# Optimization experiments

Measured on AMD Instinct MI355X. Metric: run time of the kernel, lower is better.

## Reference

```python
import jax, jax.numpy as jnp
import numpy as np

BN_EPS = 1e-5


def setup_inputs() -> dict:
    key = jax.random.key(0)
    ks = jax.random.split(key, 6)
    B, N, M, C1, C2 = 8, 8192, 2048, 128, 256
    in_ch = C1 + C2  # 384
    return {
        "xyz1": jax.random.uniform(ks[0], (B, N, 3), dtype=jnp.float32),
        "xyz2": jax.random.uniform(ks[1], (B, M, 3), dtype=jnp.float32),
        "features1": jax.random.normal(ks[2], (B, C1, N), dtype=jnp.float32),
        "features2": jax.random.normal(ks[3], (B, C2, M), dtype=jnp.float32),
        # Conv1d(kernel_size=1, bias=False) weights, squeezed to [out, in]
        "conv_w0": jax.random.normal(ks[4], (256, in_ch), dtype=jnp.float32) * 0.05,
        "gamma0": jnp.ones((256,), dtype=jnp.float32),
        "beta0": jnp.zeros((256,), dtype=jnp.float32),
        "conv_w1": jax.random.normal(ks[5], (256, 256), dtype=jnp.float32) * 0.05,
        "gamma1": jnp.ones((256,), dtype=jnp.float32),
        "beta1": jnp.zeros((256,), dtype=jnp.float32),
    }


def _conv_bn_relu(x, w, gamma, beta):
    # 1x1 Conv1d (no bias) == per-point channel matmul: [B,Cin,N] -> [B,Cout,N]
    x = jnp.einsum("oc,bcn->bon", w, x)
    # BatchNorm1d in training mode: batch stats over (B, N), biased variance
    mu = jnp.mean(x, axis=(0, 2), keepdims=True)
    var = jnp.var(x, axis=(0, 2), keepdims=True)
    x = (x - mu) * jax.lax.rsqrt(var + BN_EPS)
    x = x * gamma[None, :, None] + beta[None, :, None]
    return jax.nn.relu(x)


def reference(xyz1, xyz2, features1, features2,
              conv_w0, gamma0, beta0, conv_w1, gamma1, beta1):
    # squared pairwise distances [B, N, M] (broadcast diff reduced over coord dim)
    diff = xyz1[:, :, None, :] - xyz2[:, None, :, :]  # [B,N,M,3]
    dists = jnp.sum(diff * diff, axis=-1)             # [B,N,M]
    idx = jnp.argmin(dists, axis=-1)                  # [B,N] nearest downsampled point

    # per-batch gather: features2[b, :, idx[b]] -> [B, C2, N]
    interp = jax.vmap(lambda f, i: f[:, i])(features2, idx)

    x = jnp.concatenate([features1, interp], axis=1)  # [B, C1+C2, N]
    x = _conv_bn_relu(x, conv_w0, gamma0, beta0)
    x = _conv_bn_relu(x, conv_w1, gamma1, beta1)
    return x
```

## Files before the change

kernel.cpp:

```cpp
#include <hip/hip_runtime.h>
#include <stdint.h>

typedef unsigned short u16;
typedef unsigned int u32;
typedef __attribute__((ext_vector_type(8))) short short8;
typedef __attribute__((ext_vector_type(4))) float floatx4;

__device__ __forceinline__ u16 f2b(float f) {
  union { float f; u32 u; } c; c.f = f;
  u32 u = c.u;
  u += 0x7fffu + ((u >> 16) & 1u);
  return (u16)(u >> 16);
}
__device__ __forceinline__ float b2f(u16 h) {
  union { u32 u; float f; } c; c.u = ((u32)h) << 16;
  return c.f;
}

__device__ __forceinline__ void glds16(const void* g, void* l) {
  __builtin_amdgcn_global_load_lds((__attribute__((address_space(1))) void*)g,
                                   (__attribute__((address_space(3))) void*)l, 16, 0, 0);
}

__global__ void prep_all_k(const float* __restrict__ xyz1, const float* __restrict__ xyz2,
                           float2* __restrict__ cand,
                           const float* __restrict__ f1, u16* __restrict__ f1t,
                           const float* __restrict__ f2, u16* __restrict__ f2t,
                           const float* __restrict__ w0, u16* __restrict__ w0b,
                           const float* __restrict__ w1, u16* __restrict__ w1b,
                           float* __restrict__ sums) {
  __shared__ __align__(16) char smem[9216];
  int blk = blockIdx.x, t = threadIdx.x;
  if (blk < 512) {
    float4* s2 = (float4*)smem;
    int nq = blk & 7, mq = (blk >> 3) & 7, b = blk >> 6;
    const float* x2 = xyz2 + ((size_t)b * 2048 + mq * 256) * 3;
    s2[t] = make_float4(x2[t * 3], x2[t * 3 + 1], x2[t * 3 + 2], 0.f);
    __syncthreads();
    int n0 = nq * 1024 + t;
    float px[4], py[4], pz[4];
#pragma unroll
    for (int q = 0; q < 4; q++) {
      const float* p1 = xyz1 + ((size_t)b * 8192 + n0 + q * 256) * 3;
      px[q] = p1[0]; py[q] = p1[1]; pz[q] = p1[2];
    }
    float best[4] = {3.0e38f, 3.0e38f, 3.0e38f, 3.0e38f};
    int bi[4] = {0, 0, 0, 0};
#pragma unroll 4
    for (int m = 0; m < 256; m++) {
      float4 qq = s2[m];
#pragma unroll
      for (int q = 0; q < 4; q++) {
        float dx = px[q] - qq.x, dy = py[q] - qq.y, dz = pz[q] - qq.z;
        float d = fmaf(dz, dz, fmaf(dy, dy, dx * dx));
        bool c = d < best[q];
        best[q] = c ? d : best[q];
        bi[q] = c ? m : bi[q];
      }
    }
#pragma unroll
    for (int q = 0; q < 4; q++) {
      int n = n0 + q * 256;
      cand[(size_t)mq * 65536 + (size_t)b * 8192 + n] =
          make_float2(best[q], __int_as_float(mq * 256 + bi[q]));
    }
  } else if (blk < 3584) {
    const float* in; u16* out; int C, N, bx, by, bz;
    if (blk < 2560) { int rel = blk - 512;  in = f1; out = f1t; C = 128; N = 8192; bx = rel & 127; by = (rel >> 7) & 1; bz = rel >> 8; }
    else            { int rel = blk - 2560; in = f2; out = f2t; C = 256; N = 2048; bx = rel & 31;  by = (rel >> 5) & 3; bz = rel >> 7; }
    u16 (*tile)[72] = (u16(*)[72])smem;
    int c0 = by * 64, n0 = bx * 64;
    const float* src = in + ((size_t)bz * C + c0) * N + n0;
#pragma unroll
    for (int i = 0; i < 4; i++) {
      int id = t + i * 256;
      int c = id >> 4, nq = (id & 15) * 4;
      float4 v = *(const float4*)(src + (size_t)c * N + nq);
      tile[nq + 0][c] = f2b(v.x);
      tile[nq + 1][c] = f2b(v.y);
      tile[nq + 2][c] = f2b(v.z);
      tile[nq + 3][c] = f2b(v.w);
    }
    __syncthreads();
    int n = t >> 2, ch = (t & 3) * 16;
    u16* dst = out + ((size_t)bz * N + n0 + n) * C + c0 + ch;
    *(uint4*)dst = *(const uint4*)&tile[n][ch];
    *(uint4*)(dst + 8) = *(const uint4*)&tile[n][ch + 8];
  } else {
    int rel = blk - 3584;
    int i = rel * 256 + t;
    if (rel < 384) w0b[i] = f2b(w0[i]);
    else { int j = i - 98304; w1b[j] = f2b(w1[j]); }
    if (rel < 4) sums[i] = 0.f;
  }
}

__global__ __launch_bounds__(512) void gemm1_k(const u16* __restrict__ w0b, const u16* __restrict__ f1t,
                                               const u16* __restrict__ f2t, const float2* __restrict__ cand,
                                               float* __restrict__ sum0, float* __restrict__ sq0,
                                               u16* __restrict__ y0) {
  __shared__ u16 As[256 * 64];
  __shared__ u16 Bs[128 * 64];
  __shared__ int sidx[128];
  int t = threadIdx.x;
  int pt0 = blockIdx.x * 128;
  int b = pt0 >> 13;
  if (t < 128) {
    int p = pt0 + t;
    float bd = 3.0e38f; int bi = 0;
#pragma unroll
    for (int qc = 0; qc < 8; qc++) {
      float2 c = cand[(size_t)qc * 65536 + p];
      if (c.x < bd) { bd = c.x; bi = __float_as_int(c.y); }
    }
    sidx[t] = bi;
  }
  floatx4 zero = {0.f, 0.f, 0.f, 0.f};
  floatx4 acc[4][4];
#pragma unroll
  for (int i = 0; i < 4; i++)
#pragma unroll
    for (int j = 0; j < 4; j++) acc[i][j] = zero;
  int lane = t & 63, wave = t >> 6;
  int wrow = (wave >> 1) * 64, wcol = (wave & 1) * 64;
  int lr = lane & 15, lq = lane >> 4;
  int srow = lane >> 3;
  int sch = ((lane & 7) ^ srow) * 8;
  __syncthreads();
  int prow[2], gidx[2];
#pragma unroll
  for (int i = 0; i < 2; i++) {
    prow[i] = (wave * 2 + i) * 8 + srow;
    gidx[i] = sidx[prow[i]];
  }

#pragma unroll
  for (int k0 = 0; k0 < 384; k0 += 64) {
    __syncthreads();
#pragma unroll
    for (int i = 0; i < 4; i++) {
      int chunkA = wave * 4 + i;
      glds16(w0b + (size_t)(chunkA * 8 + srow) * 384 + k0 + sch, &As[chunkA * 512]);
    }
    if (k0 < 128) {
#pragma unroll
      for (int i = 0; i < 2; i++)
        glds16(f1t + (size_t)(pt0 + prow[i]) * 128 + k0 + sch, &Bs[(wave * 2 + i) * 512]);
    } else {
#pragma unroll
      for (int i = 0; i < 2; i++)
        glds16(f2t + ((size_t)(b << 11) + gidx[i]) * 256 + (k0 - 128) + sch, &Bs[(wave * 2 + i) * 512]);
    }
    __syncthreads();
#pragma unroll
    for (int ks = 0; ks < 2; ks++) {
      short8 af[4], bf[4];
#pragma unroll
      for (int i = 0; i < 4; i++) {
        int row = wrow + i * 16 + lr;
        af[i] = *(const short8*)&As[row * 64 + ((((ks << 2) | lq) ^ (lr & 7)) << 3)];
      }
#pragma unroll
      for (int j = 0; j < 4; j++) {
        int row = wcol + j * 16 + lr;
        bf[j] = *(const short8*)&Bs[row * 64 + ((((ks << 2) | lq) ^ (lr & 7)) << 3)];
      }
#pragma unroll
      for (int i = 0; i < 4; i++)
#pragma unroll
        for (int j = 0; j < 4; j++)
          acc[i][j] = __builtin_amdgcn_mfma_f32_16x16x32_bf16(af[i], bf[j], acc[i][j], 0, 0, 0);
    }
  }
#pragma unroll
  for (int i = 0; i < 4; i++) {
#pragma unroll
    for (int j = 0; j < 4; j++) {
      int o = wrow + i * 16 + lq * 4;
      int p = pt0 + wcol + j * 16 + lr;
      uint2 pk;
      pk.x = (u32)f2b(acc[i][j][0]) | ((u32)f2b(acc[i][j][1]) << 16);
      pk.y = (u32)f2b(acc[i][j][2]) | ((u32)f2b(acc[i][j][3]) << 16);
      *(uint2*)&y0[(size_t)p * 256 + o] = pk;
    }
  }
  __syncthreads();
  float* red = (float*)As;
  red[t] = 0.f;
  __syncthreads();
#pragma unroll
  for (int i = 0; i < 4; i++) {
#pragma unroll
    for (int r = 0; r < 4; r++) {
      float s = acc[i][0][r] + acc[i][1][r] + acc[i][2][r] + acc[i][3][r];
      float q = acc[i][0][r] * acc[i][0][r] + acc[i][1][r] * acc[i][1][r] +
                acc[i][2][r] * acc[i][2][r] + acc[i][3][r] * acc[i][3][r];
#pragma unroll
      for (int m = 8; m >= 1; m >>= 1) { s += __shfl_xor(s, m); q += __shfl_xor(q, m); }
      if (lr == 0) {
        int o = wrow + i * 16 + lq * 4 + r;
        atomicAdd(&red[o], s);
        atomicAdd(&red[256 + o], q);
      }
    }
  }
  __syncthreads();
  if (t < 256) {
    atomicAdd(&sum0[t], red[t]);
    atomicAdd(&sq0[t], red[256 + t]);
  }
}

__global__ __launch_bounds__(512) void gemm2_k(const u16* __restrict__ w1b, const u16* __restrict__ y0,
                                               const float* __restrict__ sum0, const float* __restrict__ sq0,
                                               const float* __restrict__ gamma0, const float* __restrict__ beta0,
                                               float* __restrict__ sum1, float* __restrict__ sq1,
                                               u16* __restrict__ y1) {
  __shared__ u16 As[256 * 64];
  __shared__ u16 Bs[128 * 72];
  __shared__ float ssc[256], ssh[256];
  int t = threadIdx.x;
  if (t < 256) {
    float mean = sum0[t] * (1.f / 65536.f);
    float var = fmaxf(sq0[t] * (1.f / 65536.f) - mean * mean, 0.f);
    float r = rsqrtf(var + 1e-5f);
    float sc = gamma0[t] * r;
    ssc[t] = sc;
    ssh[t] = beta0[t] - mean * sc;
  }
  int pt0 = blockIdx.x * 128;
  floatx4 zero = {0.f, 0.f, 0.f, 0.f};
  floatx4 acc[4][4];
#pragma unroll
  for (int i = 0; i < 4; i++)
#pragma unroll
    for (int j = 0; j < 4; j++) acc[i][j] = zero;
  int lane = t & 63, wave = t >> 6;
  int wrow = (wave >> 1) * 64, wcol = (wave & 1) * 64;
  int lr = lane & 15, lq = lane >> 4;
  int srow = lane >> 3;
  int sch = ((lane & 7) ^ srow) * 8;

#pragma unroll
  for (int k0 = 0; k0 < 256; k0 += 64) {
    __syncthreads();
#pragma unroll
    for (int i = 0; i < 4; i++) {
      int chunkA = wave * 4 + i;
      glds16(w1b + (size_t)(chunkA * 8 + srow) * 256 + k0 + sch, &As[chunkA * 512]);
    }
#pragma unroll
    for (int i = 0; i < 2; i++) {
      int id = t + i * 512;
      int row = id >> 3, ch = (id & 7) * 8;
      uint4 raw = *(const uint4*)(y0 + (size_t)(pt0 + row) * 256 + k0 + ch);
      u32 rw[4] = {raw.x, raw.y, raw.z, raw.w};
      u32 ow[4];
#pragma unroll
      for (int w = 0; w < 4; w++) {
        int k = k0 + ch + w * 2;
        float v0 = b2f((u16)(rw[w] & 0xffffu));
        float v1 = b2f((u16)(rw[w] >> 16));
        v0 = fmaxf(v0 * ssc[k] + ssh[k], 0.f);
        v1 = fmaxf(v1 * ssc[k + 1] + ssh[k + 1], 0.f);
        ow[w] = (u32)f2b(v0) | ((u32)f2b(v1) << 16);
      }
      uint4 ov; ov.x = ow[0]; ov.y = ow[1]; ov.z = ow[2]; ov.w = ow[3];
      *(uint4*)&Bs[row * 72 + ch] = ov;
    }
    __syncthreads();
#pragma unroll
    for (int ks = 0; ks < 2; ks++) {
      int kk = ks * 32 + lq * 8;
      short8 af[4], bf[4];
#pragma unroll
      for (int i = 0; i < 4; i++) {
        int row = wrow + i * 16 + lr;
        af[i] = *(const short8*)&As[row * 64 + ((((ks << 2) | lq) ^ (lr & 7)) << 3)];
      }
#pragma unroll
      for (int j = 0; j < 4; j++) bf[j] = *(const short8*)&Bs[(wcol + j * 16 + lr) * 72 + kk];
#pragma unroll
      for (int i = 0; i < 4; i++)
#pragma unroll
        for (int j = 0; j < 4; j++)
          acc[i][j] = __builtin_amdgcn_mfma_f32_16x16x32_bf16(af[i], bf[j], acc[i][j], 0, 0, 0);
    }
  }
#pragma unroll
  for (int i = 0; i < 4; i++) {
#pragma unroll
    for (int j = 0; j < 4; j++) {
      int o = wrow + i * 16 + lq * 4;
      int p = pt0 + wcol + j * 16 + lr;
      uint2 pk;
      pk.x = (u32)f2b(acc[i][j][0]) | ((u32)f2b(acc[i][j][1]) << 16);
      pk.y = (u32)f2b(acc[i][j][2]) | ((u32)f2b(acc[i][j][3]) << 16);
      *(uint2*)&y1[(size_t)p * 256 + o] = pk;
    }
  }
  __syncthreads();
  float* red = (float*)As;
  red[t] = 0.f;
  __syncthreads();
#pragma unroll
  for (int i = 0; i < 4; i++) {
#pragma unroll
    for (int r = 0; r < 4; r++) {
      float s = acc[i][0][r] + acc[i][1][r] + acc[i][2][r] + acc[i][3][r];
      float q = acc[i][0][r] * acc[i][0][r] + acc[i][1][r] * acc[i][1][r] +
                acc[i][2][r] * acc[i][2][r] + acc[i][3][r] * acc[i][3][r];
#pragma unroll
      for (int m = 8; m >= 1; m >>= 1) { s += __shfl_xor(s, m); q += __shfl_xor(q, m); }
      if (lr == 0) {
        int o = wrow + i * 16 + lq * 4 + r;
        atomicAdd(&red[o], s);
        atomicAdd(&red[256 + o], q);
      }
    }
  }
  __syncthreads();
  if (t < 256) {
    atomicAdd(&sum1[t], red[t]);
    atomicAdd(&sq1[t], red[256 + t]);
  }
}

__global__ void finalize_k(const u16* __restrict__ y1, const float* __restrict__ sum1,
                           const float* __restrict__ sq1, const float* __restrict__ gamma1,
                           const float* __restrict__ beta1, float* __restrict__ out) {
  __shared__ float tile[64][65];
  __shared__ float fs[64], fh[64];
  int b = blockIdx.z, o0 = blockIdx.y * 64, n0 = blockIdx.x * 64;
  int t = threadIdx.x;
  if (t < 64) {
    int o = o0 + t;
    float mean = sum1[o] * (1.f / 65536.f);
    float var = fmaxf(sq1[o] * (1.f / 65536.f) - mean * mean, 0.f);
    float r = rsqrtf(var + 1e-5f);
    float sc = gamma1[o] * r;
    fs[t] = sc;
    fh[t] = beta1[o] - mean * sc;
  }
  __syncthreads();
  int pl = t >> 2, ch = (t & 3) * 16;
  const u16* src = y1 + ((size_t)(b * 8192 + n0 + pl)) * 256 + o0 + ch;
  uint4 r0 = *(const uint4*)src;
  uint4 r1 = *(const uint4*)(src + 8);
  u16 hv[16];
  *(uint4*)&hv[0] = r0;
  *(uint4*)&hv[8] = r1;
#pragma unroll
  for (int e = 0; e < 16; e++) {
    float v = b2f(hv[e]) * fs[ch + e] + fh[ch + e];
    tile[pl][ch + e] = fmaxf(v, 0.f);
  }
  __syncthreads();
  int ol = t >> 2, nch = (t & 3) * 16;
  float* dst = out + ((size_t)(b * 256 + o0 + ol)) * 8192 + n0 + nch;
#pragma unroll
  for (int j = 0; j < 16; j += 4) {
    float4 v = make_float4(tile[nch + j][ol], tile[nch + j + 1][ol],
                           tile[nch + j + 2][ol], tile[nch + j + 3][ol]);
    *(float4*)(dst + j) = v;
  }
}

extern "C" void kernel_launch(void* const* d_in, const int* in_sizes, int n_in,
                              void* d_out, int out_size, void* d_ws, size_t ws_size,
                              hipStream_t stream) {
  const float* xyz1      = (const float*)d_in[0];
  const float* xyz2      = (const float*)d_in[1];
  const float* features1 = (const float*)d_in[2];
  const float* features2 = (const float*)d_in[3];
  const float* conv_w0   = (const float*)d_in[4];
  const float* gamma0    = (const float*)d_in[5];
  const float* beta0     = (const float*)d_in[6];
  const float* conv_w1   = (const float*)d_in[7];
  const float* gamma1    = (const float*)d_in[8];
  const float* beta1     = (const float*)d_in[9];
  float* out = (float*)d_out;

  char* ws = (char*)d_ws;
  size_t off = 0;
  auto alloc = [&](size_t bytes) {
    char* p = ws + off;
    off = (off + bytes + 4095) & ~(size_t)4095;
    return p;
  };
  float*  sums = (float*)alloc(4 * 256 * 4);
  u16*    w0b  = (u16*)alloc(256 * 384 * 2);
  u16*    w1b  = (u16*)alloc(256 * 256 * 2);
  float2* cand = (float2*)alloc((size_t)8 * 65536 * 8);
  u16*    f1t  = (u16*)alloc((size_t)65536 * 128 * 2);
  u16*    f2t  = (u16*)alloc((size_t)16384 * 256 * 2);
  u16*    y0   = (u16*)alloc((size_t)65536 * 256 * 2);
  u16*    y1   = (u16*)alloc((size_t)65536 * 256 * 2);

  prep_all_k<<<dim3(4224), 256, 0, stream>>>(xyz1, xyz2, cand, features1, f1t,
                                             features2, f2t, conv_w0, w0b, conv_w1, w1b, sums);
  gemm1_k<<<dim3(512), 512, 0, stream>>>(w0b, f1t, f2t, cand, sums + 0, sums + 256, y0);
  gemm2_k<<<dim3(512), 512, 0, stream>>>(w1b, y0, sums + 0, sums + 256, gamma0, beta0,
                                         sums + 512, sums + 768, y1);
  finalize_k<<<dim3(128, 4, 8), 256, 0, stream>>>(y1, sums + 512, sums + 768, gamma1, beta1, out);
}
```

Before: 243.5 us.

## Shrink GEMM tiles to 64 points with 4-wave blocks for more occupancy

Both GEMM kernels now use 256-thread blocks covering 64 points instead of 512-thread blocks covering 128, with each wave owning 64 output channels across all 64 points. Grid size doubles to 1024 and launch bounds request 4 blocks per CU, to get more blocks across CUs and better latency hiding. Each wave now computes its own nearest-neighbour indices, which removes the shared index array and a barrier. The channel statistics use plain shared stores instead of shared atomics, since each channel now has a single writer. gemm2's B tile switches from padded rows to an XOR-swizzled layout. In exchange, the weight tile is reloaded twice as often per point and twice as many global atomics are issued for the stats.

```diff
diff --git a/kernel.cpp b/kernel.cpp
--- a/kernel.cpp
+++ b/kernel.cpp
@@ -95,25 +95,31 @@
   }
 }
 
-__global__ __launch_bounds__(512) void gemm1_k(const u16* __restrict__ w0b, const u16* __restrict__ f1t,
-                                               const u16* __restrict__ f2t, const float2* __restrict__ cand,
-                                               float* __restrict__ sum0, float* __restrict__ sq0,
-                                               u16* __restrict__ y0) {
+__global__ __launch_bounds__(256, 4) void gemm1_k(const u16* __restrict__ w0b, const u16* __restrict__ f1t,
+                                                  const u16* __restrict__ f2t, const float2* __restrict__ cand,
+                                                  float* __restrict__ sum0, float* __restrict__ sq0,
+                                                  u16* __restrict__ y0) {
   __shared__ u16 As[256 * 64];
-  __shared__ u16 Bs[128 * 64];
-  __shared__ int sidx[128];
+  __shared__ u16 Bs[64 * 64];
   int t = threadIdx.x;
-  int pt0 = blockIdx.x * 128;
+  int pt0 = blockIdx.x * 64;
   int b = pt0 >> 13;
-  if (t < 128) {
-    int p = pt0 + t;
+  int lane = t & 63, wave = t >> 6;
+  int wrow = wave * 64;
+  int lr = lane & 15, lq = lane >> 4;
+  int srow = lane >> 3;
+  int sch = ((lane & 7) ^ srow) * 8;
+  int gidx[2];
+#pragma unroll
+  for (int i = 0; i < 2; i++) {
+    int p = pt0 + (wave * 2 + i) * 8 + srow;
     float bd = 3.0e38f; int bi = 0;
 #pragma unroll
     for (int qc = 0; qc < 8; qc++) {
       float2 c = cand[(size_t)qc * 65536 + p];
       if (c.x < bd) { bd = c.x; bi = __float_as_int(c.y); }
     }
-    sidx[t] = bi;
+    gidx[i] = bi;
   }
   floatx4 zero = {0.f, 0.f, 0.f, 0.f};
   floatx4 acc[4][4];
@@ -121,35 +127,25 @@
   for (int i = 0; i < 4; i++)
 #pragma unroll
     for (int j = 0; j < 4; j++) acc[i][j] = zero;
-  int lane = t & 63, wave = t >> 6;
-  int wrow = (wave >> 1) * 64, wcol = (wave & 1) * 64;
-  int lr = lane & 15, lq = lane >> 4;
-  int srow = lane >> 3;
-  int sch = ((lane & 7) ^ srow) * 8;
-  __syncthreads();
-  int prow[2], gidx[2];
-#pragma unroll
-  for (int i = 0; i < 2; i++) {
-    prow[i] = (wave * 2 + i) * 8 + srow;
-    gidx[i] = sidx[prow[i]];
-  }
 
 #pragma unroll
   for (int k0 = 0; k0 < 384; k0 += 64) {
     __syncthreads();
 #pragma unroll
-    for (int i = 0; i < 4; i++) {
-      int chunkA = wave * 4 + i;
-      glds16(w0b + (size_t)(chunkA * 8 + srow) * 384 + k0 + sch, &As[chunkA * 512]);
+    for (int i = 0; i < 8; i++) {
+      int chunk = wave * 8 + i;
+      glds16(w0b + (size_t)(chunk * 8 + srow) * 384 + k0 + sch, &As[chunk * 512]);
     }
     if (k0 < 128) {
 #pragma unroll
       for (int i = 0; i < 2; i++)
-        glds16(f1t + (size_t)(pt0 + prow[i]) * 128 + k0 + sch, &Bs[(wave * 2 + i) * 512]);
+        glds16(f1t + (size_t)(pt0 + (wave * 2 + i) * 8 + srow) * 128 + k0 + sch,
+               &Bs[(wave * 2 + i) * 512]);
     } else {
 #pragma unroll
       for (int i = 0; i < 2; i++)
-        glds16(f2t + ((size_t)(b << 11) + gidx[i]) * 256 + (k0 - 128) + sch, &Bs[(wave * 2 + i) * 512]);
+        glds16(f2t + ((size_t)(b << 11) + gidx[i]) * 256 + (k0 - 128) + sch,
+               &Bs[(wave * 2 + i) * 512]);
     }
     __syncthreads();
 #pragma unroll
@@ -162,7 +158,7 @@
       }
 #pragma unroll
       for (int j = 0; j < 4; j++) {
-        int row = wcol + j * 16 + lr;
+        int row = j * 16 + lr;
         bf[j] = *(const short8*)&Bs[row * 64 + ((((ks << 2) | lq) ^ (lr & 7)) << 3)];
       }
 #pragma unroll
@@ -177,7 +173,7 @@
 #pragma unroll
     for (int j = 0; j < 4; j++) {
       int o = wrow + i * 16 + lq * 4;
-      int p = pt0 + wcol + j * 16 + lr;
+      int p = pt0 + j * 16 + lr;
       uint2 pk;
       pk.x = (u32)f2b(acc[i][j][0]) | ((u32)f2b(acc[i][j][1]) << 16);
       pk.y = (u32)f2b(acc[i][j][2]) | ((u32)f2b(acc[i][j][3]) << 16);
@@ -186,8 +182,6 @@
   }
   __syncthreads();
   float* red = (float*)As;
-  red[t] = 0.f;
-  __syncthreads();
 #pragma unroll
   for (int i = 0; i < 4; i++) {
 #pragma unroll
@@ -199,28 +193,26 @@
       for (int m = 8; m >= 1; m >>= 1) { s += __shfl_xor(s, m); q += __shfl_xor(q, m); }
       if (lr == 0) {
         int o = wrow + i * 16 + lq * 4 + r;
-        atomicAdd(&red[o], s);
-        atomicAdd(&red[256 + o], q);
-      }
-    }
-  }
-  __syncthreads();
-  if (t < 256) {
-    atomicAdd(&sum0[t], red[t]);
-    atomicAdd(&sq0[t], red[256 + t]);
-  }
-}
-
-__global__ __launch_bounds__(512) void gemm2_k(const u16* __restrict__ w1b, const u16* __restrict__ y0,
-                                               const float* __restrict__ sum0, const float* __restrict__ sq0,
-                                               const float* __restrict__ gamma0, const float* __restrict__ beta0,
-                                               float* __restrict__ sum1, float* __restrict__ sq1,
-                                               u16* __restrict__ y1) {
+        red[o] = s;
+        red[256 + o] = q;
+      }
+    }
+  }
+  __syncthreads();
+  atomicAdd(&sum0[t], red[t]);
+  atomicAdd(&sq0[t], red[256 + t]);
+}
+
+__global__ __launch_bounds__(256, 4) void gemm2_k(const u16* __restrict__ w1b, const u16* __restrict__ y0,
+                                                  const float* __restrict__ sum0, const float* __restrict__ sq0,
+                                                  const float* __restrict__ gamma0, const float* __restrict__ beta0,
+                                                  float* __restrict__ sum1, float* __restrict__ sq1,
+                                                  u16* __restrict__ y1) {
   __shared__ u16 As[256 * 64];
-  __shared__ u16 Bs[128 * 72];
+  __shared__ u16 Bs[64 * 64];
   __shared__ float ssc[256], ssh[256];
   int t = threadIdx.x;
-  if (t < 256) {
+  {
     float mean = sum0[t] * (1.f / 65536.f);
     float var = fmaxf(sq0[t] * (1.f / 65536.f) - mean * mean, 0.f);
     float r = rsqrtf(var + 1e-5f);
@@ -228,7 +220,7 @@
     ssc[t] = sc;
     ssh[t] = beta0[t] - mean * sc;
   }
-  int pt0 = blockIdx.x * 128;
+  int pt0 = blockIdx.x * 64;
   floatx4 zero = {0.f, 0.f, 0.f, 0.f};
   floatx4 acc[4][4];
 #pragma unroll
@@ -236,7 +228,7 @@
 #pragma unroll
     for (int j = 0; j < 4; j++) acc[i][j] = zero;
   int lane = t & 63, wave = t >> 6;
-  int wrow = (wave >> 1) * 64, wcol = (wave & 1) * 64;
+  int wrow = wave * 64;
   int lr = lane & 15, lq = lane >> 4;
   int srow = lane >> 3;
   int sch = ((lane & 7) ^ srow) * 8;
@@ -245,14 +237,15 @@
   for (int k0 = 0; k0 < 256; k0 += 64) {
     __syncthreads();
 #pragma unroll
-    for (int i = 0; i < 4; i++) {
-      int chunkA = wave * 4 + i;
-      glds16(w1b + (size_t)(chunkA * 8 + srow) * 256 + k0 + sch, &As[chunkA * 512]);
+    for (int i = 0; i < 8; i++) {
+      int chunk = wave * 8 + i;
+      glds16(w1b + (size_t)(chunk * 8 + srow) * 256 + k0 + sch, &As[chunk * 512]);
     }
 #pragma unroll
     for (int i = 0; i < 2; i++) {
-      int id = t + i * 512;
-      int row = id >> 3, ch = (id & 7) * 8;
+      int id = t + i * 256;
+      int row = id >> 3, pc = id & 7;
+      int ch = ((pc ^ (row & 7)) * 8);
       uint4 raw = *(const uint4*)(y0 + (size_t)(pt0 + row) * 256 + k0 + ch);
       u32 rw[4] = {raw.x, raw.y, raw.z, raw.w};
       u32 ow[4];
@@ -266,12 +259,11 @@
         ow[w] = (u32)f2b(v0) | ((u32)f2b(v1) << 16);
       }
       uint4 ov; ov.x = ow[0]; ov.y = ow[1]; ov.z = ow[2]; ov.w = ow[3];
-      *(uint4*)&Bs[row * 72 + ch] = ov;
+      *(uint4*)&Bs[row * 64 + pc * 8] = ov;
     }
     __syncthreads();
 #pragma unroll
     for (int ks = 0; ks < 2; ks++) {
-      int kk = ks * 32 + lq * 8;
       short8 af[4], bf[4];
 #pragma unroll
       for (int i = 0; i < 4; i++) {
@@ -279,7 +271,10 @@
         af[i] = *(const short8*)&As[row * 64 + ((((ks << 2) | lq) ^ (lr & 7)) << 3)];
       }
 #pragma unroll
-      for (int j = 0; j < 4; j++) bf[j] = *(const short8*)&Bs[(wcol + j * 16 + lr) * 72 + kk];
+      for (int j = 0; j < 4; j++) {
+        int row = j * 16 + lr;
+        bf[j] = *(const short8*)&Bs[row * 64 + ((((ks << 2) | lq) ^ (lr & 7)) << 3)];
+      }
 #pragma unroll
       for (int i = 0; i < 4; i++)
 #pragma unroll
@@ -292,7 +287,7 @@
 #pragma unroll
     for (int j = 0; j < 4; j++) {
       int o = wrow + i * 16 + lq * 4;
-      int p = pt0 + wcol + j * 16 + lr;
+      int p = pt0 + j * 16 + lr;
       uint2 pk;
       pk.x = (u32)f2b(acc[i][j][0]) | ((u32)f2b(acc[i][j][1]) << 16);
       pk.y = (u32)f2b(acc[i][j][2]) | ((u32)f2b(acc[i][j][3]) << 16);
@@ -301,8 +296,6 @@
   }
   __syncthreads();
   float* red = (float*)As;
-  red[t] = 0.f;
-  __syncthreads();
 #pragma unroll
   for (int i = 0; i < 4; i++) {
 #pragma unroll
@@ -314,16 +307,14 @@
       for (int m = 8; m >= 1; m >>= 1) { s += __shfl_xor(s, m); q += __shfl_xor(q, m); }
       if (lr == 0) {
         int o = wrow + i * 16 + lq * 4 + r;
-        atomicAdd(&red[o], s);
-        atomicAdd(&red[256 + o], q);
-      }
-    }
-  }
-  __syncthreads();
-  if (t < 256) {
-    atomicAdd(&sum1[t], red[t]);
-    atomicAdd(&sq1[t], red[256 + t]);
-  }
+        red[o] = s;
+        red[256 + o] = q;
+      }
+    }
+  }
+  __syncthreads();
+  atomicAdd(&sum1[t], red[t]);
+  atomicAdd(&sq1[t], red[256 + t]);
 }
 
 __global__ void finalize_k(const u16* __restrict__ y1, const float* __restrict__ sum1,
@@ -399,8 +390,8 @@
 
   prep_all_k<<<dim3(4224), 256, 0, stream>>>(xyz1, xyz2, cand, features1, f1t,
                                              features2, f2t, conv_w0, w0b, conv_w1, w1b, sums);
-  gemm1_k<<<dim3(512), 512, 0, stream>>>(w0b, f1t, f2t, cand, sums + 0, sums + 256, y0);
-  gemm2_k<<<dim3(512), 512, 0, stream>>>(w1b, y0, sums + 0, sums + 256, gamma0, beta0,
-                                         sums + 512, sums + 768, y1);
+  gemm1_k<<<dim3(1024), 256, 0, stream>>>(w0b, f1t, f2t, cand, sums + 0, sums + 256, y0);
+  gemm2_k<<<dim3(1024), 256, 0, stream>>>(w1b, y0, sums + 0, sums + 256, gamma0, beta0,
+                                          sums + 512, sums + 768, y1);
   finalize_k<<<dim3(128, 4, 8), 256, 0, stream>>>(y1, sums + 512, sums + 768, gamma1, beta1, out);
 }
```

Result: slower. 250.3 us (+2.8%).
